# Kernel tuning notes

Hardware: AMD Instinct MI355X
Metric: run time of the kernel (lower is better)

## Reference

```python
import jax, jax.numpy as jnp
import numpy as np

RATIOS = np.array([0.5, 1.0, 2.0], np.float32)
SCALES = np.array([8.0, 16.0, 32.0], np.float32)
IMAGE_SIZE = 1920.0
UPPER, LOWER = 0.4, 0.1
NPOS_MAX, NNEG_MAX = 128, 60   # sample_num=256 -> bg_num = min(60, 256-npos) = 60
BETA = 0.1
EPS = 1e-6


def make_anchors(H, W, stride):
    # K = len(RATIOS)*len(SCALES) anchors per grid cell, sizes stride*scale, aspect per ratio
    ws = (stride * SCALES[None, :] * np.sqrt(1.0 / RATIOS[:, None])).reshape(-1)  # [K]
    hs = (stride * SCALES[None, :] * np.sqrt(RATIOS[:, None])).reshape(-1)        # [K]
    cx = (np.arange(W, dtype=np.float32) + 0.5) * stride
    cy = (np.arange(H, dtype=np.float32) + 0.5) * stride
    cxg, cyg = np.meshgrid(cx, cy)  # [H, W]
    a = np.stack([cxg[..., None] - ws / 2, cyg[..., None] - hs / 2,
                  cxg[..., None] + ws / 2, cyg[..., None] + hs / 2], axis=-1)  # [H, W, K, 4]
    return jnp.asarray(a, jnp.float32)


def pairwise_iou(b, g):
    # b: [A, 4], g: [M, 4] -> [A, M]
    ab = jnp.maximum(b[:, 2] - b[:, 0], 0.0) * jnp.maximum(b[:, 3] - b[:, 1], 0.0)
    ag = jnp.maximum(g[:, 2] - g[:, 0], 0.0) * jnp.maximum(g[:, 3] - g[:, 1], 0.0)
    x1 = jnp.maximum(b[:, None, 0], g[None, :, 0])
    y1 = jnp.maximum(b[:, None, 1], g[None, :, 1])
    x2 = jnp.minimum(b[:, None, 2], g[None, :, 2])
    y2 = jnp.minimum(b[:, None, 3], g[None, :, 3])
    inter = jnp.maximum(x2 - x1, 0.0) * jnp.maximum(y2 - y1, 0.0)
    return inter / (ab[:, None] + ag[None, :] - inter + EPS)


def encode(box, anchor):
    # standard (tx, ty, tw, th) box encoding relative to anchor
    aw = anchor[:, 2] - anchor[:, 0]; ah = anchor[:, 3] - anchor[:, 1]
    acx = anchor[:, 0] + 0.5 * aw; acy = anchor[:, 1] + 0.5 * ah
    bw = jnp.maximum(box[:, 2] - box[:, 0], EPS); bh = jnp.maximum(box[:, 3] - box[:, 1], EPS)
    bcx = box[:, 0] + 0.5 * bw; bcy = box[:, 1] + 0.5 * bh
    return jnp.stack([(bcx - acx) / aw, (bcy - acy) / ah,
                      jnp.log(bw / aw), jnp.log(bh / ah)], axis=-1)


def smooth_l1(d):
    ad = jnp.abs(d)
    return jnp.where(ad < BETA, 0.5 * d * d / BETA, ad - 0.5 * BETA)


def per_image(regions, cls, gt, key, anchors_flat, n_norm):
    iou = pairwise_iou(regions, gt)                       # [A, M]
    best = iou.max(axis=1)
    arg = iou.argmax(axis=1).astype(jnp.int32)
    # match(): >= upper -> gt index (positive), < lower -> NEGATIVE(-1), else ignore(-2)
    matches = jnp.where(best >= UPPER, arg, jnp.where(best < LOWER, -1, -2))
    kp, kn = jax.random.split(key)
    # randperm-style sampling without replacement: top_k over random scores on masked anchors
    pos_score = jnp.where(matches >= 0, jax.random.uniform(kp, matches.shape), -1.0)
    pv, pidx = jax.lax.top_k(pos_score, NPOS_MAX)
    pvalid = (pv > 0.0).astype(jnp.float32)               # npos = min(num_pos, 128)
    neg_score = jnp.where(matches == -1, jax.random.uniform(kn, matches.shape), -1.0)
    nv, nidx = jax.lax.top_k(neg_score, NNEG_MAX)
    nvalid = (nv > 0.0).astype(jnp.float32)
    npos = pvalid.sum(); nneg = nvalid.sum()
    lp = cls[pidx]; ln = cls[nidx]
    # BCEWithLogits(mean): label 1 -> softplus(-x), label 0 -> softplus(x)
    bce = jnp.sum(jax.nn.softplus(-lp) * pvalid) + jnp.sum(jax.nn.softplus(ln) * nvalid)
    denom = jnp.maximum(npos + nneg, 1.0)
    cls_loss = bce / denom
    gt_sel = gt[jnp.clip(matches[pidx], 0, gt.shape[0] - 1)]
    anc = anchors_flat[pidx]
    tp = encode(regions[pidx], anc)
    tg = encode(gt_sel, anc)
    l1 = smooth_l1(tp - tg).sum(-1)                       # [NPOS_MAX]
    bbox_loss = jnp.sum(l1 * pvalid) / (jnp.maximum(npos, 1.0) * n_norm)
    pred_mean = (jnp.sum(lp * pvalid) + jnp.sum(ln * nvalid)) / denom
    return cls_loss, bbox_loss, npos, nneg, pred_mean


def reference(cls_scores, bbox_deltas, gt_boxes):
    N, K, H, W = cls_scores.shape
    stride = round(IMAGE_SIZE / W)
    anc = make_anchors(H, W, stride)                      # [H, W, K, 4]
    deltas = bbox_deltas.transpose(0, 2, 3, 1).reshape(N, H, W, K, 4)
    # regions = anchors + deltas, cross_boundary(remove=False) -> clip to image
    regions = jnp.clip(anc[None] + deltas, 0.0, IMAGE_SIZE).reshape(N, -1, 4)
    cls = cls_scores.transpose(0, 2, 3, 1).reshape(N, -1)
    keys = jax.random.split(jax.random.key(42), N)
    cl, bl, fg, bg, pm = jax.vmap(per_image, in_axes=(0, 0, 0, 0, None, None))(
        regions, cls, gt_boxes, keys, anc.reshape(-1, 4), float(N))
    return (cl.sum(), bl.sum(), bg.sum(), fg.sum(), pm[-1])


def setup_inputs():
    key = jax.random.key(0)
    k1, k2, k3, k4 = jax.random.split(key, 4)
    N, K, H, W, M = 8, 9, 120, 120, 64
    cls_scores = jax.random.normal(k1, (N, K, H, W), jnp.float32)
    bbox_deltas = jax.random.normal(k2, (N, 4 * K, H, W), jnp.float32) * 4.0
    xy = jax.random.uniform(k3, (N, M, 2), jnp.float32) * 1500.0
    wh = jax.random.uniform(k4, (N, M, 2), jnp.float32) * 360.0 + 40.0
    gt_boxes = jnp.concatenate([xy, xy + wh], axis=-1)    # valid [x1,y1,x2,y2] in-image
    return {"cls_scores": cls_scores, "bbox_deltas": bbox_deltas, "gt_boxes": gt_boxes}
```

## Files before the change

### kernel.cpp

```cpp
#include <hip/hip_runtime.h>
#include <stdint.h>

#define N_IMG 8
#define K_ANC 9
#define HW_G  14400
#define W_G   120
#define A_TOT 129600
#define M_GT  64
#define NBIN  1024
#define CAP   2048
#define NSUB  8

#define POISON_U32 0xAAAAAAAAu

static constexpr size_t OFF_PHIST = 0;
static constexpr size_t OFF_NHIST = 32768;
static constexpr size_t OFF_CNT   = 65536;
static constexpr size_t OFF_THR   = 65600;
static constexpr size_t OFF_DONE  = 65856;
static constexpr size_t OFF_ACC   = 65920;
static constexpr size_t OFF_ENT   = 67584;
static constexpr size_t OFF_BND   = OFF_ENT + 4ull * N_IMG * A_TOT;

__device__ __forceinline__ uint32_t rotl32(uint32_t v, int r) {
  return (v << r) | (v >> (32 - r));
}

__device__ void tf2x32(uint32_t k0, uint32_t k1, uint32_t x0, uint32_t x1,
                       uint32_t& o0, uint32_t& o1) {
  uint32_t ks2 = 0x1BD11BDAu ^ k0 ^ k1;
  x0 += k0; x1 += k1;
#define TF_R(r) { x0 += x1; x1 = rotl32(x1, r); x1 ^= x0; }
  TF_R(13) TF_R(15) TF_R(26) TF_R(6)
  x0 += k1; x1 += ks2 + 1u;
  TF_R(17) TF_R(29) TF_R(16) TF_R(24)
  x0 += ks2; x1 += k0 + 2u;
  TF_R(13) TF_R(15) TF_R(26) TF_R(6)
  x0 += k0; x1 += k1 + 3u;
  TF_R(17) TF_R(29) TF_R(16) TF_R(24)
  x0 += k1; x1 += ks2 + 4u;
  TF_R(13) TF_R(15) TF_R(26) TF_R(6)
  x0 += ks2; x1 += k0 + 5u;
#undef TF_R
  o0 = x0; o1 = x1;
}

constexpr uint64_t tf_c(uint32_t k0, uint32_t k1, uint32_t x0, uint32_t x1) {
  const int R[20] = {13,15,26,6,17,29,16,24,13,15,26,6,17,29,16,24,13,15,26,6};
  uint32_t ks[3] = {k0, k1, 0x1BD11BDAu ^ k0 ^ k1};
  x0 += k0; x1 += k1;
  for (int r = 0; r < 20; ++r) {
    x0 += x1; x1 = (x1 << R[r]) | (x1 >> (32 - R[r])); x1 ^= x0;
    if ((r & 3) == 3) {
      int d = r / 4 + 1;
      x0 += ks[d % 3]; x1 += ks[(d + 1) % 3] + (uint32_t)d;
    }
  }
  return ((uint64_t)x0 << 32) | x1;
}

struct KeyTab { uint32_t v[N_IMG][4]; };
constexpr KeyTab make_keys() {
  KeyTab K{};
  for (int n = 0; n < N_IMG; ++n) {
    uint64_t f = tf_c(0u, 42u, 0u, (uint32_t)n);
    uint32_t i0 = (uint32_t)(f >> 32), i1 = (uint32_t)f;
    uint64_t p = tf_c(i0, i1, 0u, 0u);
    uint64_t q = tf_c(i0, i1, 0u, 1u);
    K.v[n][0] = (uint32_t)(p >> 32); K.v[n][1] = (uint32_t)p;
    K.v[n][2] = (uint32_t)(q >> 32); K.v[n][3] = (uint32_t)q;
  }
  return K;
}
__constant__ KeyTab KEYS = make_keys();

__device__ void acc_pos(int n, int l, int m, const float* __restrict__ cls,
                        const float* __restrict__ del, const float* __restrict__ gt,
                        float& sp, float& pr, float& l1s) {
  int k = l / HW_G, hw = l - k * HW_G;
  const float scales[3] = {8.f, 16.f, 32.f};
  const float ratios[3] = {0.5f, 1.f, 2.f};
  float sc = scales[k % 3], rt = ratios[k / 3];
  float wsz = (16.f * sc) * sqrtf(1.f / rt);
  float hsz = (16.f * sc) * sqrtf(rt);
  int w = hw % W_G, h = hw / W_G;
  float cx = ((float)w + 0.5f) * 16.f, cy = ((float)h + 0.5f) * 16.f;
  float ax1 = cx - wsz * 0.5f, ay1 = cy - hsz * 0.5f;
  float ax2 = cx + wsz * 0.5f, ay2 = cy + hsz * 0.5f;
  int base = (n * 36 + k * 4) * HW_G + hw;
  float rx1 = fminf(fmaxf(ax1 + del[base], 0.f), 1920.f);
  float ry1 = fminf(fmaxf(ay1 + del[base + HW_G], 0.f), 1920.f);
  float rx2 = fminf(fmaxf(ax2 + del[base + 2 * HW_G], 0.f), 1920.f);
  float ry2 = fminf(fmaxf(ay2 + del[base + 3 * HW_G], 0.f), 1920.f);
  float L = cls[n * A_TOT + l];
  sp += fmaxf(-L, 0.f) + log1pf(expf(-fabsf(L)));
  pr += L;
  const float* g = gt + (n * M_GT + m) * 4;
  float aw = ax2 - ax1, ah = ay2 - ay1;
  float acx = ax1 + 0.5f * aw, acy = ay1 + 0.5f * ah;
  float bw = fmaxf(rx2 - rx1, 1e-6f), bh = fmaxf(ry2 - ry1, 1e-6f);
  float bcx = rx1 + 0.5f * bw, bcy = ry1 + 0.5f * bh;
  float gw = fmaxf(g[2] - g[0], 1e-6f), gh = fmaxf(g[3] - g[1], 1e-6f);
  float gcx = g[0] + 0.5f * gw, gcy = g[1] + 0.5f * gh;
  float dd[4];
  dd[0] = (bcx - acx) / aw - (gcx - acx) / aw;
  dd[1] = (bcy - acy) / ah - (gcy - acy) / ah;
  dd[2] = logf(bw / aw) - logf(gw / aw);
  dd[3] = logf(bh / ah) - logf(gh / ah);
  float t = 0.f;
  for (int i = 0; i < 4; ++i) {
    float ad = fabsf(dd[i]);
    t += (ad < 0.1f) ? (0.5f * dd[i] * dd[i] / 0.1f) : (ad - 0.05f);
  }
  l1s += t;
}

__device__ void acc_neg(int n, int l, const float* __restrict__ cls,
                        float& sp, float& pr) {
  float L = cls[n * A_TOT + l];
  sp += fmaxf(L, 0.f) + log1pf(expf(-fabsf(L)));
  pr += L;
}

__device__ void reduce3_atomic(float sp, float pr, float l1, float* accf, int n,
                               int tid) {
  __shared__ float swv[3][4];
  float v0 = sp, v1 = pr, v2 = l1;
  for (int off = 32; off > 0; off >>= 1) {
    v0 += __shfl_down(v0, off); v1 += __shfl_down(v1, off); v2 += __shfl_down(v2, off);
  }
  int wv = tid >> 6, ln = tid & 63;
  if (ln == 0) { swv[0][wv] = v0; swv[1][wv] = v1; swv[2][wv] = v2; }
  __syncthreads();
  if (tid == 0) {
    atomicAdd(&accf[n * 48 + 0],  swv[0][0] + swv[0][1] + swv[0][2] + swv[0][3]);
    atomicAdd(&accf[n * 48 + 16], swv[1][0] + swv[1][1] + swv[1][2] + swv[1][3]);
    atomicAdd(&accf[n * 48 + 32], swv[2][0] + swv[2][1] + swv[2][2] + swv[2][3]);
  }
  __syncthreads();
}

__global__ __launch_bounds__(64) void k_match(
    const float* __restrict__ del, const float* __restrict__ gt, uint8_t* ws) {
  const int k = blockIdx.y, n = blockIdx.z;
  const int tid = threadIdx.x;
  const int hw = blockIdx.x * 64 + tid;
  __shared__ float4 cbox[M_GT];
  __shared__ float car[M_GT];
  __shared__ int cidx[M_GT];

  float4 g4 = reinterpret_cast<const float4*>(gt)[n * M_GT + tid];

  const float scales[3] = {8.f, 16.f, 32.f};
  const float ratios[3] = {0.5f, 1.f, 2.f};
  float sc = scales[k % 3], rt = ratios[k / 3];
  float wsz = (16.f * sc) * sqrtf(1.f / rt);
  float hsz = (16.f * sc) * sqrtf(rt);
  int w = hw % W_G, h = hw / W_G;
  float cx = ((float)w + 0.5f) * 16.f, cy = ((float)h + 0.5f) * 16.f;
  float ax1 = cx - wsz * 0.5f, ay1 = cy - hsz * 0.5f;
  float ax2 = cx + wsz * 0.5f, ay2 = cy + hsz * 0.5f;
  const float* dp = del + (size_t)(n * 36 + k * 4) * HW_G + hw;
  float rx1 = fminf(fmaxf(ax1 + dp[0], 0.f), 1920.f);
  float ry1 = fminf(fmaxf(ay1 + dp[HW_G], 0.f), 1920.f);
  float rx2 = fminf(fmaxf(ax2 + dp[2 * HW_G], 0.f), 1920.f);
  float ry2 = fminf(fmaxf(ay2 + dp[3 * HW_G], 0.f), 1920.f);
  float ab = fmaxf(rx2 - rx1, 0.f) * fmaxf(ry2 - ry1, 0.f);

  float xmn = rx1, xmx = rx2, ymn = ry1, ymx = ry2;
  for (int off = 32; off > 0; off >>= 1) {
    xmn = fminf(xmn, __shfl_xor(xmn, off));
    xmx = fmaxf(xmx, __shfl_xor(xmx, off));
    ymn = fminf(ymn, __shfl_xor(ymn, off));
    ymx = fmaxf(ymx, __shfl_xor(ymx, off));
  }
  bool keep = (g4.x < xmx) && (g4.z > xmn) && (g4.y < ymx) && (g4.w > ymn);
  unsigned long long mk = __ballot(keep);
  int Mp = __popcll(mk);
  if (keep) {
    int pos = __popcll(mk & ((1ull << tid) - 1ull));
    cbox[pos] = g4;
    car[pos] = fmaxf(g4.z - g4.x, 0.f) * fmaxf(g4.w - g4.y, 0.f);
    cidx[pos] = tid;
  }

  float ib = -1.f, ub = 1.f;
  int arg = 0;
  for (int j = 0; j < Mp; ++j) {
    float4 b = cbox[j];
    float ga = car[j];
    int oj = cidx[j];
    float ix1 = fmaxf(rx1, b.x), iy1 = fmaxf(ry1, b.y);
    float ix2 = fminf(rx2, b.z), iy2 = fminf(ry2, b.w);
    float inter = fmaxf(ix2 - ix1, 0.f) * fmaxf(iy2 - iy1, 0.f);
    float u = ab + ga - inter + 1e-6f;
    bool gc = (inter * ub) > (ib * u);
    ib = gc ? inter : ib;
    ub = gc ? u : ub;
    arg = gc ? oj : arg;
  }
  float best = ib / ub;
  int m = (best >= 0.4f) ? arg : ((best < 0.1f) ? -1 : -2);

  uint32_t a32 = (uint32_t)(hw * 9 + k);
  uint32_t sk0 = (m >= 0) ? KEYS.v[n][0] : KEYS.v[n][2];
  uint32_t sk1 = (m >= 0) ? KEYS.v[n][1] : KEYS.v[n][3];
  uint32_t y0, y1;
  tf2x32(sk0, sk1, 0u, a32, y0, y1);
  uint32_t bits = (y0 ^ y1) >> 9;

  uint32_t e = 0u;
  if (bits) {
    if (m >= 0)       e = 0x80000000u | ((uint32_t)m << 23) | bits;
    else if (m == -1) e = bits;
  }
  ((uint32_t*)(ws + OFF_ENT))[(size_t)n * A_TOT + (size_t)k * HW_G + hw] = e;
  if (e) {
    uint32_t* hist = (uint32_t*)(ws + OFF_PHIST);
    uint32_t off = (e >> 31) ? 0u : (uint32_t)(N_IMG * NBIN);
    atomicAdd(&hist[off + n * NBIN + (bits >> 13)], 1u);
  }
}

__global__ __launch_bounds__(256) void k_scan(
    const float* __restrict__ cls, const float* __restrict__ del,
    const float* __restrict__ gt, uint8_t* ws) {
  const int sub = blockIdx.x, which = blockIdx.y, n = blockIdx.z;
  const int tid = threadIdx.x;
  const uint32_t* hist = (const uint32_t*)(ws + OFF_PHIST);
  const uint32_t* ent = (const uint32_t*)(ws + OFF_ENT);
  uint32_t* cnt = (uint32_t*)(ws + OFF_CNT);
  int* thrg = (int*)(ws + OFF_THR);
  unsigned long long* bnd = (unsigned long long*)(ws + OFF_BND);
  float* accf = (float*)(ws + OFF_ACC);

  __shared__ uint32_t shist[NBIN];
  __shared__ uint32_t chunk[256];
  __shared__ int tb[3];

  const uint32_t* hsrc = hist + (which ? (size_t)N_IMG * NBIN : 0) + n * NBIN;
  for (int i = tid; i < NBIN; i += 256) shist[i] = hsrc[i] - POISON_U32;
  __syncthreads();
  chunk[tid] = shist[tid * 4] + shist[tid * 4 + 1] +
               shist[tid * 4 + 2] + shist[tid * 4 + 3];
  __syncthreads();
  if (tid == 0) {
    int kk = (which == 0) ? 128 : 60;
    unsigned c = 0; int b = -1; int need = 0;
    for (int t = 255; t >= 0; --t) {
      unsigned cc = chunk[t];
      if (c + cc >= (unsigned)kk) {
        for (int i = t * 4 + 3;; --i) {
          unsigned hc = shist[i];
          if (c + hc >= (unsigned)kk) { b = i; need = kk - (int)c; break; }
          c += hc;
        }
        break;
      }
      c += cc;
    }
    tb[0] = b; tb[1] = need; tb[2] = (b < 0) ? (int)c : kk;
  }
  __syncthreads();
  if (sub == 0 && tid < 3) thrg[n * 6 + which * 3 + tid] = tb[tid];

  const int bB = tb[0];
  float sp = 0.f, pr = 0.f, l1 = 0.f;
  const uint32_t* en = ent + (size_t)n * A_TOT;
  for (int it = 0; it < 16; ++it) {
    int l0 = sub * 16384 + it * 1024 + tid * 4;
    if (l0 >= A_TOT) break;
    uint4 e4 = *reinterpret_cast<const uint4*>(en + l0);
    uint32_t ev[4] = {e4.x, e4.y, e4.z, e4.w};
#pragma unroll
    for (int j = 0; j < 4; ++j) {
      uint32_t e = ev[j];
      if (!e) continue;
      bool isPos = (e >> 31) != 0u;
      if ((which == 0) != isPos) continue;
      int l = l0 + j;
      uint32_t bits = e & 0x7FFFFFu;
      int bin = (int)(bits >> 13);
      if (bin > bB) {
        if (isPos) acc_pos(n, l, (int)((e >> 23) & 0x3Fu), cls, del, gt, sp, pr, l1);
        else       acc_neg(n, l, cls, sp, pr);
      } else if (bin == bB) {
        int i = (int)(atomicAdd(&cnt[n * 2 + which], 1u) - POISON_U32);
        if (i < CAP) {
          int k = l / HW_G, hw = l - k * HW_G, a = hw * 9 + k;
          bnd[(size_t)(n * 2 + which) * CAP + i] =
              ((unsigned long long)bits << 17) | (unsigned)(0x1FFFF - a);
        }
      }
    }
  }
  reduce3_atomic(sp, pr, l1, accf, n, tid);
}

__global__ __launch_bounds__(256) void k_bound_out(
    const float* __restrict__ cls, const float* __restrict__ del,
    const float* __restrict__ gt, float* __restrict__ out, uint8_t* ws) {
  const int which = blockIdx.x, n = blockIdx.y, tid = threadIdx.x;
  const uint32_t* ent = (const uint32_t*)(ws + OFF_ENT);
  const int* thr = (const int*)(ws + OFF_THR);
  const uint32_t* cnt = (const uint32_t*)(ws + OFF_CNT);
  const unsigned long long* bnd =
      (const unsigned long long*)(ws + OFF_BND) + (size_t)(n * 2 + which) * CAP;
  float* accf = (float*)(ws + OFF_ACC);
  uint32_t* done = (uint32_t*)(ws + OFF_DONE);
  __shared__ int sLast;

  int need = thr[n * 6 + which * 3 + 1];
  float sp = 0.f, pr = 0.f, l1 = 0.f;
  if (need > 0) {
    __shared__ unsigned long long sb[CAP];
    int m = min((int)(cnt[n * 2 + which] - POISON_U32), CAP);
    for (int i = tid; i < m; i += 256) sb[i] = bnd[i];
    __syncthreads();
    for (int i = tid; i < m; i += 256) {
      unsigned long long key = sb[i];
      int rank = 0;
      for (int j = 0; j < m; ++j) rank += (sb[j] > key) ? 1 : 0;
      if (rank < need) {
        int a = 0x1FFFF - (int)(key & 0x1FFFFull);
        int k = a % 9, hw = a / 9;
        int l = k * HW_G + hw;
        if (which == 0) {
          uint32_t e = ent[(size_t)n * A_TOT + l];
          acc_pos(n, l, (int)((e >> 23) & 0x3Fu), cls, del, gt, sp, pr, l1);
        } else {
          acc_neg(n, l, cls, sp, pr);
        }
      }
    }
    __syncthreads();
  }
  reduce3_atomic(sp, pr, l1, accf, n, tid);

  __threadfence();
  if (tid == 0)
    sLast = (atomicAdd(done, 1u) == POISON_U32 + 2u * N_IMG - 1u) ? 1 : 0;
  __syncthreads();
  if (!sLast) return;
  __threadfence();

  if (tid == 0) {
    const float PF = __uint_as_float(POISON_U32);
    const int* thrr = (const int*)(ws + OFF_THR);
    float c = 0.f, b = 0.f, fg = 0.f, bg = 0.f, pm = 0.f;
    for (int nn = 0; nn < N_IMG; ++nn) {
      float npos = (float)thrr[nn * 6 + 2];
      float nneg = (float)thrr[nn * 6 + 5];
      float denom = fmaxf(npos + nneg, 1.f);
      c += (accf[nn * 48 + 0] - PF) / denom;
      b += (accf[nn * 48 + 32] - PF) / (fmaxf(npos, 1.f) * 8.0f);
      fg += npos; bg += nneg;
      if (nn == N_IMG - 1) pm = (accf[nn * 48 + 16] - PF) / denom;
    }
    out[0] = c; out[1] = b; out[2] = bg; out[3] = fg; out[4] = pm;
  }
}

extern "C" void kernel_launch(void* const* d_in, const int* in_sizes, int n_in,
                              void* d_out, int out_size, void* d_ws, size_t ws_size,
                              hipStream_t stream) {
  (void)in_sizes; (void)n_in; (void)out_size; (void)ws_size;
  const float* cls = (const float*)d_in[0];
  const float* del = (const float*)d_in[1];
  const float* gt  = (const float*)d_in[2];
  float* out = (float*)d_out;
  uint8_t* ws = (uint8_t*)d_ws;

  hipLaunchKernelGGL(k_match, dim3(HW_G / 64, K_ANC, N_IMG), dim3(64), 0, stream,
                     del, gt, ws);
  hipLaunchKernelGGL(k_scan, dim3(NSUB, 2, N_IMG), dim3(256), 0, stream,
                     cls, del, gt, ws);
  hipLaunchKernelGGL(k_bound_out, dim3(2, N_IMG), dim3(256), 0, stream,
                     cls, del, gt, out, ws);
}
```

Before: 136.2 us.

## Fuse scan and boundary kernels, pack four wave-windows per match block

```diff
diff --git a/kernel.cpp b/kernel.cpp
--- a/kernel.cpp
+++ b/kernel.cpp
@@ -9,7 +9,9 @@
 #define M_GT  64
 #define NBIN  1024
 #define CAP   2048
-#define NSUB  8
+#define WIN_TOT 2025
+#define WPB   4
+#define NSUB2 32
 
 #define POISON_U32 0xAAAAAAAAu
 
@@ -140,16 +142,20 @@
   __syncthreads();
 }
 
-__global__ __launch_bounds__(64) void k_match(
+__global__ __launch_bounds__(256) void k_match(
     const float* __restrict__ del, const float* __restrict__ gt, uint8_t* ws) {
-  const int k = blockIdx.y, n = blockIdx.z;
+  const int n = blockIdx.y;
   const int tid = threadIdx.x;
-  const int hw = blockIdx.x * 64 + tid;
-  __shared__ float4 cbox[M_GT];
-  __shared__ float car[M_GT];
-  __shared__ int cidx[M_GT];
-
-  float4 g4 = reinterpret_cast<const float4*>(gt)[n * M_GT + tid];
+  const int wid = tid >> 6, ln = tid & 63;
+  const int win = blockIdx.x * WPB + wid;
+  __shared__ float4 cbox[WPB][M_GT];
+  __shared__ float car[WPB][M_GT];
+  __shared__ int cidx[WPB][M_GT];
+  if (win >= WIN_TOT) return;
+  const int k = win / 225;
+  const int hw = (win - k * 225) * 64 + ln;
+
+  float4 g4 = reinterpret_cast<const float4*>(gt)[n * M_GT + ln];
 
   const float scales[3] = {8.f, 16.f, 32.f};
   const float ratios[3] = {0.5f, 1.f, 2.f};
@@ -178,18 +184,18 @@
   unsigned long long mk = __ballot(keep);
   int Mp = __popcll(mk);
   if (keep) {
-    int pos = __popcll(mk & ((1ull << tid) - 1ull));
-    cbox[pos] = g4;
-    car[pos] = fmaxf(g4.z - g4.x, 0.f) * fmaxf(g4.w - g4.y, 0.f);
-    cidx[pos] = tid;
+    int pos = __popcll(mk & ((1ull << ln) - 1ull));
+    cbox[wid][pos] = g4;
+    car[wid][pos] = fmaxf(g4.z - g4.x, 0.f) * fmaxf(g4.w - g4.y, 0.f);
+    cidx[wid][pos] = ln;
   }
 
   float ib = -1.f, ub = 1.f;
   int arg = 0;
   for (int j = 0; j < Mp; ++j) {
-    float4 b = cbox[j];
-    float ga = car[j];
-    int oj = cidx[j];
+    float4 b = cbox[wid][j];
+    float ga = car[wid][j];
+    int oj = cidx[wid][j];
     float ix1 = fmaxf(rx1, b.x), iy1 = fmaxf(ry1, b.y);
     float ix2 = fminf(rx2, b.z), iy2 = fminf(ry2, b.w);
     float inter = fmaxf(ix2 - ix1, 0.f) * fmaxf(iy2 - iy1, 0.f);
@@ -222,10 +228,10 @@
   }
 }
 
-__global__ __launch_bounds__(256) void k_scan(
+__global__ __launch_bounds__(256) void k_scan_bound(
     const float* __restrict__ cls, const float* __restrict__ del,
-    const float* __restrict__ gt, uint8_t* ws) {
-  const int sub = blockIdx.x, which = blockIdx.y, n = blockIdx.z;
+    const float* __restrict__ gt, float* __restrict__ out, uint8_t* ws) {
+  const int sub = blockIdx.x, n = blockIdx.y;
   const int tid = threadIdx.x;
   const uint32_t* hist = (const uint32_t*)(ws + OFF_PHIST);
   const uint32_t* ent = (const uint32_t*)(ws + OFF_ENT);
@@ -233,43 +239,61 @@
   int* thrg = (int*)(ws + OFF_THR);
   unsigned long long* bnd = (unsigned long long*)(ws + OFF_BND);
   float* accf = (float*)(ws + OFF_ACC);
-
-  __shared__ uint32_t shist[NBIN];
-  __shared__ uint32_t chunk[256];
-  __shared__ int tb[3];
-
-  const uint32_t* hsrc = hist + (which ? (size_t)N_IMG * NBIN : 0) + n * NBIN;
-  for (int i = tid; i < NBIN; i += 256) shist[i] = hsrc[i] - POISON_U32;
+  uint32_t* done_img = (uint32_t*)(ws + OFF_DONE);
+  uint32_t* done_fin = (uint32_t*)(ws + OFF_DONE + 32);
+
+  __shared__ unsigned long long sb[CAP];
+  uint32_t* shist = (uint32_t*)sb;
+  uint32_t* sfx = ((uint32_t*)sb) + 2 * NBIN;
+  __shared__ int tbv[2][3];
+  __shared__ int sLast, sFin;
+
+  {
+    const uint32_t* hp = hist + n * NBIN;
+    const uint32_t* hn = hist + (size_t)N_IMG * NBIN + n * NBIN;
+    for (int i = tid; i < NBIN; i += 256) {
+      shist[i] = hp[i] - POISON_U32;
+      shist[NBIN + i] = hn[i] - POISON_U32;
+    }
+  }
   __syncthreads();
-  chunk[tid] = shist[tid * 4] + shist[tid * 4 + 1] +
-               shist[tid * 4 + 2] + shist[tid * 4 + 3];
-  __syncthreads();
-  if (tid == 0) {
-    int kk = (which == 0) ? 128 : 60;
-    unsigned c = 0; int b = -1; int need = 0;
-    for (int t = 255; t >= 0; --t) {
-      unsigned cc = chunk[t];
-      if (c + cc >= (unsigned)kk) {
-        for (int i = t * 4 + 3;; --i) {
-          unsigned hc = shist[i];
-          if (c + hc >= (unsigned)kk) { b = i; need = kk - (int)c; break; }
+  for (int wq = 0; wq < 2; ++wq) {
+    const uint32_t* sh = shist + wq * NBIN;
+    uint32_t cs = sh[tid * 4] + sh[tid * 4 + 1] + sh[tid * 4 + 2] + sh[tid * 4 + 3];
+    sfx[tid] = cs;
+    __syncthreads();
+    for (int off = 1; off < 256; off <<= 1) {
+      uint32_t v = (tid + off < 256) ? sfx[tid + off] : 0u;
+      __syncthreads();
+      sfx[tid] += v;
+      __syncthreads();
+    }
+    const uint32_t kk = wq ? 60u : 128u;
+    if (sfx[0] < kk) {
+      if (tid == 0) { tbv[wq][0] = -1; tbv[wq][1] = 0; tbv[wq][2] = (int)sfx[0]; }
+    } else {
+      uint32_t above = (tid == 255) ? 0u : sfx[tid + 1];
+      if (sfx[tid] >= kk && above < kk) {
+        uint32_t c = above;
+        for (int i = tid * 4 + 3;; --i) {
+          uint32_t hc = sh[i];
+          if (c + hc >= kk) {
+            tbv[wq][0] = i; tbv[wq][1] = (int)(kk - c); tbv[wq][2] = (int)kk;
+            break;
+          }
           c += hc;
         }
-        break;
       }
-      c += cc;
-    }
-    tb[0] = b; tb[1] = need; tb[2] = (b < 0) ? (int)c : kk;
-  }
-  __syncthreads();
-  if (sub == 0 && tid < 3) thrg[n * 6 + which * 3 + tid] = tb[tid];
-
-  const int bB = tb[0];
+    }
+    __syncthreads();
+  }
+
+  const int bBp = tbv[0][0], bBn = tbv[1][0];
   float sp = 0.f, pr = 0.f, l1 = 0.f;
   const uint32_t* en = ent + (size_t)n * A_TOT;
-  for (int it = 0; it < 16; ++it) {
-    int l0 = sub * 16384 + it * 1024 + tid * 4;
-    if (l0 >= A_TOT) break;
+  for (int it = 0; it < 4; ++it) {
+    int l0 = sub * 4096 + it * 1024 + tid * 4;
+    if (l0 >= A_TOT) continue;
     uint4 e4 = *reinterpret_cast<const uint4*>(en + l0);
     uint32_t ev[4] = {e4.x, e4.y, e4.z, e4.w};
 #pragma unroll
@@ -277,7 +301,7 @@
       uint32_t e = ev[j];
       if (!e) continue;
       bool isPos = (e >> 31) != 0u;
-      if ((which == 0) != isPos) continue;
+      int bB = isPos ? bBp : bBn;
       int l = l0 + j;
       uint32_t bits = e & 0x7FFFFFu;
       int bin = (int)(bits >> 13);
@@ -285,63 +309,62 @@
         if (isPos) acc_pos(n, l, (int)((e >> 23) & 0x3Fu), cls, del, gt, sp, pr, l1);
         else       acc_neg(n, l, cls, sp, pr);
       } else if (bin == bB) {
-        int i = (int)(atomicAdd(&cnt[n * 2 + which], 1u) - POISON_U32);
+        int wq = isPos ? 0 : 1;
+        int i = (int)(atomicAdd(&cnt[n * 2 + wq], 1u) - POISON_U32);
         if (i < CAP) {
           int k = l / HW_G, hw = l - k * HW_G, a = hw * 9 + k;
-          bnd[(size_t)(n * 2 + which) * CAP + i] =
+          bnd[(size_t)(n * 2 + wq) * CAP + i] =
               ((unsigned long long)bits << 17) | (unsigned)(0x1FFFF - a);
         }
       }
     }
   }
+  __threadfence();
   reduce3_atomic(sp, pr, l1, accf, n, tid);
-}
-
-__global__ __launch_bounds__(256) void k_bound_out(
-    const float* __restrict__ cls, const float* __restrict__ del,
-    const float* __restrict__ gt, float* __restrict__ out, uint8_t* ws) {
-  const int which = blockIdx.x, n = blockIdx.y, tid = threadIdx.x;
-  const uint32_t* ent = (const uint32_t*)(ws + OFF_ENT);
-  const int* thr = (const int*)(ws + OFF_THR);
-  const uint32_t* cnt = (const uint32_t*)(ws + OFF_CNT);
-  const unsigned long long* bnd =
-      (const unsigned long long*)(ws + OFF_BND) + (size_t)(n * 2 + which) * CAP;
-  float* accf = (float*)(ws + OFF_ACC);
-  uint32_t* done = (uint32_t*)(ws + OFF_DONE);
-  __shared__ int sLast;
-
-  int need = thr[n * 6 + which * 3 + 1];
-  float sp = 0.f, pr = 0.f, l1 = 0.f;
-  if (need > 0) {
-    __shared__ unsigned long long sb[CAP];
-    int m = min((int)(cnt[n * 2 + which] - POISON_U32), CAP);
-    for (int i = tid; i < m; i += 256) sb[i] = bnd[i];
-    __syncthreads();
-    for (int i = tid; i < m; i += 256) {
-      unsigned long long key = sb[i];
-      int rank = 0;
-      for (int j = 0; j < m; ++j) rank += (sb[j] > key) ? 1 : 0;
-      if (rank < need) {
-        int a = 0x1FFFF - (int)(key & 0x1FFFFull);
-        int k = a % 9, hw = a / 9;
-        int l = k * HW_G + hw;
-        if (which == 0) {
-          uint32_t e = ent[(size_t)n * A_TOT + l];
-          acc_pos(n, l, (int)((e >> 23) & 0x3Fu), cls, del, gt, sp, pr, l1);
-        } else {
-          acc_neg(n, l, cls, sp, pr);
+
+  if (tid == 0)
+    sLast = (atomicAdd(&done_img[n], 1u) == POISON_U32 + NSUB2 - 1u) ? 1 : 0;
+  __syncthreads();
+  if (!sLast) return;
+  __threadfence();
+
+  if (tid < 6) thrg[n * 6 + tid] = ((const int*)tbv)[tid];
+
+  float sp2 = 0.f, pr2 = 0.f, l12 = 0.f;
+  for (int wq = 0; wq < 2; ++wq) {
+    int need = tbv[wq][1];
+    if (need > 0) {
+      __syncthreads();
+      int m = min((int)(cnt[n * 2 + wq] - POISON_U32), CAP);
+      const unsigned long long* bq = bnd + (size_t)(n * 2 + wq) * CAP;
+      for (int i = tid; i < m; i += 256) sb[i] = bq[i];
+      __syncthreads();
+      for (int i = tid; i < m; i += 256) {
+        unsigned long long key = sb[i];
+        int rank = 0;
+        for (int j = 0; j < m; ++j) rank += (sb[j] > key) ? 1 : 0;
+        if (rank < need) {
+          int a = 0x1FFFF - (int)(key & 0x1FFFFull);
+          int k = a % 9, hw = a / 9;
+          int l = k * HW_G + hw;
+          if (wq == 0) {
+            uint32_t e = ent[(size_t)n * A_TOT + l];
+            acc_pos(n, l, (int)((e >> 23) & 0x3Fu), cls, del, gt, sp2, pr2, l12);
+          } else {
+            acc_neg(n, l, cls, sp2, pr2);
+          }
         }
       }
-    }
-    __syncthreads();
-  }
-  reduce3_atomic(sp, pr, l1, accf, n, tid);
+      __syncthreads();
+    }
+  }
+  reduce3_atomic(sp2, pr2, l12, accf, n, tid);
 
   __threadfence();
   if (tid == 0)
-    sLast = (atomicAdd(done, 1u) == POISON_U32 + 2u * N_IMG - 1u) ? 1 : 0;
+    sFin = (atomicAdd(done_fin, 1u) == POISON_U32 + N_IMG - 1u) ? 1 : 0;
   __syncthreads();
-  if (!sLast) return;
+  if (!sFin) return;
   __threadfence();
 
   if (tid == 0) {
@@ -371,10 +394,8 @@
   float* out = (float*)d_out;
   uint8_t* ws = (uint8_t*)d_ws;
 
-  hipLaunchKernelGGL(k_match, dim3(HW_G / 64, K_ANC, N_IMG), dim3(64), 0, stream,
-                     del, gt, ws);
-  hipLaunchKernelGGL(k_scan, dim3(NSUB, 2, N_IMG), dim3(256), 0, stream,
-                     cls, del, gt, ws);
-  hipLaunchKernelGGL(k_bound_out, dim3(2, N_IMG), dim3(256), 0, stream,
+  hipLaunchKernelGGL(k_match, dim3((WIN_TOT + WPB - 1) / WPB, N_IMG), dim3(256),
+                     0, stream, del, gt, ws);
+  hipLaunchKernelGGL(k_scan_bound, dim3(NSUB2, N_IMG), dim3(256), 0, stream,
                      cls, del, gt, out, ws);
 }
```

After: 140.4 us. 3.1% more time.
